# Kernel optimization log

Measured on AMD Instinct MI355X. Metric: run time of the kernel, lower is better.

## Reference

```python
import jax, jax.numpy as jnp
import numpy as np

T, N, R = 10, 50000, 50000   # time steps, nodes per graph, total restaurants
D_IN, D, H = 128, 64, 4      # input dim, hidden dim, attention heads
E = 400000                   # edges per timestep (before self-loops)
HD = D // H                  # head dim


def setup_inputs() -> dict:
    key = jax.random.key(0)
    ks = jax.random.split(key, 16)
    inp = {}
    inp["x"] = jax.random.normal(ks[0], (T, N, D_IN), jnp.float32)
    inp["edge_index"] = jax.random.randint(ks[1], (T, 2, E), 0, N, jnp.int32)
    inp["edge_weight"] = jax.random.uniform(ks[2], (T, E), jnp.float32)
    # per-timestep permutation mapping local node idx -> global restaurant idx
    inp["global_idx"] = jax.vmap(lambda k: jax.random.permutation(k, R))(
        jax.random.split(ks[3], T)).astype(jnp.int32)
    s = 0.05
    inp["gcn1_w"] = jax.random.normal(ks[4], (D, D_IN), jnp.float32) * s
    inp["gcn1_b"] = jnp.zeros((D,), jnp.float32)
    inp["gcn2_w"] = jax.random.normal(ks[5], (D, D), jnp.float32) * s
    inp["gcn2_b"] = jnp.zeros((D,), jnp.float32)
    inp["in_proj_w"] = jax.random.normal(ks[6], (3 * D, D), jnp.float32) * s
    inp["in_proj_b"] = jnp.zeros((3 * D,), jnp.float32)
    inp["out_proj_w"] = jax.random.normal(ks[7], (D, D), jnp.float32) * s
    inp["out_proj_b"] = jnp.zeros((D,), jnp.float32)
    inp["w1"] = jnp.ones((T, D), jnp.float32)
    inp["w2"] = jnp.ones((T, D), jnp.float32)
    inp["w3"] = jnp.ones((D,), jnp.float32)
    inp["w4"] = jnp.ones((D,), jnp.float32)
    inp["ln1_g"] = jnp.ones((D,), jnp.float32)
    inp["ln1_b"] = jnp.zeros((D,), jnp.float32)
    inp["ln2_g"] = jnp.ones((D,), jnp.float32)
    inp["ln2_b"] = jnp.zeros((D,), jnp.float32)
    inp["fc_w"] = jax.random.normal(ks[8], (D, D), jnp.float32) * s
    inp["fc_b"] = jnp.zeros((D,), jnp.float32)
    return inp


def _layer_norm(x, g, b, eps=1e-5):
    mu = jnp.mean(x, axis=-1, keepdims=True)
    var = jnp.mean((x - mu) ** 2, axis=-1, keepdims=True)
    return (x - mu) * jax.lax.rsqrt(var + eps) * g + b


def _gcn_layer(h, src, dst, ew, W, b):
    # PyG GCNConv with edge weights; self-loops already appended by caller.
    deg = jax.ops.segment_sum(ew, dst, num_segments=N)
    dinv = jnp.where(deg > 0, jax.lax.rsqrt(deg), 0.0)
    norm = dinv[src] * ew * dinv[dst]                      # [E+N]
    hw = h @ W.T                                           # [N, D]
    agg = jax.ops.segment_sum(norm[:, None] * hw[src], dst, num_segments=N)
    return agg + b


def _forward(x, edge_index, edge_weight, global_idx,
             gcn1_w, gcn1_b, gcn2_w, gcn2_b,
             in_proj_w, in_proj_b, out_proj_w, out_proj_b,
             w1, w2, w3, w4, ln1_g, ln1_b, ln2_g, ln2_b, fc_w, fc_b):
    loop = jnp.arange(N, dtype=edge_index.dtype)
    src = jnp.concatenate([edge_index[:, 0], jnp.broadcast_to(loop, (T, N))], axis=1)
    dst = jnp.concatenate([edge_index[:, 1], jnp.broadcast_to(loop, (T, N))], axis=1)
    ew = jnp.concatenate([edge_weight, jnp.ones((T, N), edge_weight.dtype)], axis=1)

    def per_t(xt, st, dt, wt):
        h = jax.nn.relu(_gcn_layer(xt, st, dt, wt, gcn1_w, gcn1_b))
        return jax.nn.relu(_gcn_layer(h, st, dt, wt, gcn2_w, gcn2_b))

    feat = jax.vmap(per_t)(x, src, dst, ew)                # [T, N, D]

    # scatter local features to global alignment (permutation per timestep)
    aligned = jax.vmap(lambda g, f: jnp.zeros((R, D), f.dtype).at[g].set(f))(
        global_idx, feat)                                  # [T, R, D]
    time_embeds = jnp.transpose(aligned, (1, 0, 2))        # [R, T, D]

    presence = jax.vmap(
        lambda g: jnp.zeros((R,), bool).at[g].set(True))(global_idx)  # [T, R]
    key_padding_mask = ~presence.T                          # [R, T], True = ignore
    bias = jnp.where(key_padding_mask, -1e9, 0.0)           # [R, T]

    # multi-head self-attention over time axis (batch_first, batch = R)
    qkv = time_embeds @ in_proj_w.T + in_proj_b             # [R, T, 3D]
    q, k, v = jnp.split(qkv, 3, axis=-1)
    q = q.reshape(R, T, H, HD)
    k = k.reshape(R, T, H, HD)
    v = v.reshape(R, T, H, HD)
    scores = jnp.einsum('rthd,rshd->rhts', q, k) / np.sqrt(HD)
    scores = scores + bias[:, None, None, :]
    attn = jax.nn.softmax(scores, axis=-1)                  # [R, H, T, T]
    ao = jnp.einsum('rhts,rshd->rthd', attn, v).reshape(R, T, D)
    attn_out = ao @ out_proj_w.T + out_proj_b               # [R, T, D]

    # dropouts are identity in eval mode
    time_feat = _layer_norm(w1 * time_embeds + w2 * attn_out, ln1_g, ln1_b)
    final = time_feat[:, -1, :]                             # [R, D]
    out = final @ fc_w.T + fc_b                             # [R, D]
    return _layer_norm(w3 * final + w4 * out, ln2_g, ln2_b)


def reference(x, edge_index, edge_weight, global_idx,
              gcn1_w, gcn1_b, gcn2_w, gcn2_b,
              in_proj_w, in_proj_b, out_proj_w, out_proj_b,
              w1, w2, w3, w4, ln1_g, ln1_b, ln2_g, ln2_b, fc_w, fc_b):
    return _forward(x, edge_index, edge_weight, global_idx,
                    gcn1_w, gcn1_b, gcn2_w, gcn2_b,
                    in_proj_w, in_proj_b, out_proj_w, out_proj_b,
                    w1, w2, w3, w4, ln1_g, ln1_b, ln2_g, ln2_b, fc_w, fc_b)
```

## Files before the change

kernel.cpp:

```cpp
#include <hip/hip_runtime.h>
#include <cstdint>
#include <cstddef>

namespace {

constexpr int T = 10;
constexpr int N = 50000;
constexpr int R = 50000;
constexpr int DIN = 128;
constexpr int D = 64;
constexpr int E = 400000;

constexpr int BINS = 8192;
constexpr int NR = 7;
constexpr int SEG = 16;
constexpr int ESEG = E / SEG;
constexpr int EV4 = ESEG / 4;

constexpr float WSCALE = 262144.0f;
constexpr float WINV = 1.0f / 262144.0f;

typedef __attribute__((ext_vector_type(8))) short bf16x8;
typedef __attribute__((ext_vector_type(4))) float f32x4;

__device__ __forceinline__ float bf2f(unsigned short u) {
  return __uint_as_float(((unsigned)u) << 16);
}
__device__ __forceinline__ unsigned short f2bf(float f) {
  unsigned u = __float_as_uint(f);
  return (unsigned short)((u + 0x7FFFu + ((u >> 16) & 1u)) >> 16);
}

__global__ __launch_bounds__(256) void k_hist(const int* __restrict__ ei,
                                              const float* __restrict__ ew,
                                              unsigned* __restrict__ pu) {
  __shared__ unsigned h[BINS];
  int b = blockIdx.x;
  int s = b % SEG;
  int tr = b / SEG;
  int r = tr % NR;
  int t = tr / NR;
  for (int i = threadIdx.x; i < BINS; i += 256) h[i] = 0u;
  __syncthreads();
  int bin0 = r * BINS;
  const int4* dst4 = (const int4*)(ei + (size_t)t * 2 * E + E + s * ESEG);
  const float4* ew4 = (const float4*)(ew + (size_t)t * E + s * ESEG);
  for (int i = threadIdx.x; i < EV4; i += 256) {
    int4 d = dst4[i];
    float4 w = ew4[i];
    unsigned a0 = (unsigned)(d.x - bin0);
    unsigned a1 = (unsigned)(d.y - bin0);
    unsigned a2 = (unsigned)(d.z - bin0);
    unsigned a3 = (unsigned)(d.w - bin0);
    if (a0 < (unsigned)BINS) atomicAdd(&h[a0], 0x1000000u + (unsigned)fmaf(w.x, WSCALE, 0.5f));
    if (a1 < (unsigned)BINS) atomicAdd(&h[a1], 0x1000000u + (unsigned)fmaf(w.y, WSCALE, 0.5f));
    if (a2 < (unsigned)BINS) atomicAdd(&h[a2], 0x1000000u + (unsigned)fmaf(w.z, WSCALE, 0.5f));
    if (a3 < (unsigned)BINS) atomicAdd(&h[a3], 0x1000000u + (unsigned)fmaf(w.w, WSCALE, 0.5f));
  }
  __syncthreads();
  size_t base = (size_t)b * BINS;
  for (int i = threadIdx.x; i < BINS; i += 256) pu[base + i] = h[i];
}

__global__ __launch_bounds__(256) void k_hreduce(const unsigned* __restrict__ pu,
                                                 int* __restrict__ cnt,
                                                 float* __restrict__ dinv) {
  int i = blockIdx.x * 256 + threadIdx.x;
  if (i >= T * N) return;
  int t = i / N, n = i - t * N;
  int r = n / BINS, rel = n - r * BINS;
  unsigned c = 0;
  unsigned wsum = 0;
  #pragma unroll
  for (int s = 0; s < SEG; ++s) {
    unsigned v = pu[((size_t)((t * NR + r) * SEG + s)) * BINS + rel];
    c += v >> 24;
    wsum += v & 0xFFFFFFu;
  }
  cnt[i] = (int)c;
  dinv[i] = rsqrtf(1.0f + (float)wsum * WINV);
}

__global__ __launch_bounds__(256) void k_scan(const int* __restrict__ cnt,
                                              int* __restrict__ rowptr) {
  int t = blockIdx.x;
  int lane = threadIdx.x & 63, wid = threadIdx.x >> 6;
  __shared__ int wsum[4];
  __shared__ int carry_s;
  if (threadIdx.x == 0) carry_s = 0;
  __syncthreads();
  const int4* cp = (const int4*)(cnt + (size_t)t * N);
  int4* rp = (int4*)(rowptr + (size_t)t * N);
  constexpr int NI4 = N / 4;
  for (int base = 0; base < NI4; base += 256) {
    int i = base + threadIdx.x;
    int4 v = make_int4(0, 0, 0, 0);
    if (i < NI4) v = cp[i];
    int tot = v.x + v.y + v.z + v.w;
    int s = tot;
    #pragma unroll
    for (int off = 1; off < 64; off <<= 1) {
      int u = __shfl_up(s, off, 64);
      if (lane >= off) s += u;
    }
    if (lane == 63) wsum[wid] = s;
    int carry = carry_s;
    __syncthreads();
    int wadd = 0;
    #pragma unroll
    for (int w = 0; w < 4; ++w) if (w < wid) wadd += wsum[w];
    if (i < NI4) {
      int excl = carry + wadd + s - tot;
      int4 o;
      o.x = excl;
      o.y = excl + v.x;
      o.z = o.y + v.y;
      o.w = o.z + v.z;
      rp[i] = o;
    }
    __syncthreads();
    if (threadIdx.x == 0) carry_s = carry + wsum[0] + wsum[1] + wsum[2] + wsum[3];
    __syncthreads();
  }
}

__global__ __launch_bounds__(256) void k_segoff(unsigned* __restrict__ pu,
                                                const int* __restrict__ rowptr) {
  int i = blockIdx.x * 256 + threadIdx.x;
  if (i >= T * N) return;
  int t = i / N, n = i - t * N;
  int r = n / BINS, rel = n - r * BINS;
  unsigned run = (unsigned)rowptr[i];
  #pragma unroll
  for (int s = 0; s < SEG; ++s) {
    size_t base = ((size_t)((t * NR + r) * SEG + s)) * BINS + rel;
    unsigned v = pu[base];
    pu[base] = run;
    run += v >> 24;
  }
}

__global__ __launch_bounds__(256) void k_fill2(const int* __restrict__ ei,
                                               const float* __restrict__ ew,
                                               const unsigned* __restrict__ pu,
                                               int2* __restrict__ pk) {
  __shared__ int cur[BINS];
  int b = blockIdx.x;
  int s = b % SEG;
  int tr = b / SEG;
  int r = tr % NR;
  int t = tr / NR;
  size_t pbase = (size_t)b * BINS;
  for (int i = threadIdx.x; i < BINS; i += 256) cur[i] = (int)pu[pbase + i];
  __syncthreads();
  int bin0 = r * BINS;
  const int4* src4 = (const int4*)(ei + (size_t)t * 2 * E + s * ESEG);
  const int4* dst4 = (const int4*)(ei + (size_t)t * 2 * E + E + s * ESEG);
  const float4* ew4 = (const float4*)(ew + (size_t)t * E + s * ESEG);
  int2* pkt = pk + (size_t)t * E;
  for (int i = threadIdx.x; i < EV4; i += 256) {
    int4 d = dst4[i];
    int4 sv = src4[i];
    float4 w = ew4[i];
    unsigned a0 = (unsigned)(d.x - bin0);
    unsigned a1 = (unsigned)(d.y - bin0);
    unsigned a2 = (unsigned)(d.z - bin0);
    unsigned a3 = (unsigned)(d.w - bin0);
    if (a0 < (unsigned)BINS) {
      int pos = atomicAdd(&cur[a0], 1);
      pkt[pos] = make_int2(sv.x, __float_as_int(w.x));
    }
    if (a1 < (unsigned)BINS) {
      int pos = atomicAdd(&cur[a1], 1);
      pkt[pos] = make_int2(sv.y, __float_as_int(w.y));
    }
    if (a2 < (unsigned)BINS) {
      int pos = atomicAdd(&cur[a2], 1);
      pkt[pos] = make_int2(sv.z, __float_as_int(w.z));
    }
    if (a3 < (unsigned)BINS) {
      int pos = atomicAdd(&cur[a3], 1);
      pkt[pos] = make_int2(sv.w, __float_as_int(w.w));
    }
  }
}

__global__ __launch_bounds__(256) void k_prep(const float* __restrict__ g1w,
                                              const float* __restrict__ g2w,
                                              const float* __restrict__ inw,
                                              const float* __restrict__ outw,
                                              const float* __restrict__ fcw,
                                              unsigned short* __restrict__ Wb) {
  int i = blockIdx.x * 256 + threadIdx.x;
  if (i >= 32768) return;
  const float* src;
  int off;
  if (i < 8192)       { src = g1w;  off = 0; }
  else if (i < 12288) { src = g2w;  off = 8192; }
  else if (i < 24576) { src = inw;  off = 12288; }
  else if (i < 28672) { src = outw; off = 24576; }
  else                { src = fcw;  off = 28672; }
  Wb[i] = f2bf(src[i - off]);
}

template <int K, int NT, bool BF16B, int MODE>
__global__ __launch_bounds__(256) void k_mm(const unsigned short* __restrict__ Wb,
                                            const void* __restrict__ Bv,
                                            const float* __restrict__ biasp,
                                            unsigned short* __restrict__ out,
                                            unsigned short* __restrict__ q9,
                                            int Mwaves) {
  int wv = threadIdx.x >> 6, lane = threadIdx.x & 63;
  int wave = blockIdx.x * 4 + wv;
  if (wave >= Mwaves) return;
  int m0 = wave * 16;
  int half = lane & 15, quad = lane >> 4;
  constexpr int KS = K / 32;
  int m = m0 + half;
  float ds = 1.0f;
  if (MODE == 2) ds = biasp[m];
  bf16x8 bfrag[KS];
  if (BF16B) {
    const unsigned short* Bp = (const unsigned short*)Bv + (size_t)m * K + quad * 8;
    #pragma unroll
    for (int ks = 0; ks < KS; ++ks) bfrag[ks] = *(const bf16x8*)(Bp + ks * 32);
  } else {
    const float* Bp = (const float*)Bv + (size_t)m * K + quad * 8;
    #pragma unroll
    for (int ks = 0; ks < KS; ++ks) {
      float4 f0 = *(const float4*)(Bp + ks * 32);
      float4 f1 = *(const float4*)(Bp + ks * 32 + 4);
      bf16x8 b;
      b[0] = (short)f2bf(f0.x); b[1] = (short)f2bf(f0.y);
      b[2] = (short)f2bf(f0.z); b[3] = (short)f2bf(f0.w);
      b[4] = (short)f2bf(f1.x); b[5] = (short)f2bf(f1.y);
      b[6] = (short)f2bf(f1.z); b[7] = (short)f2bf(f1.w);
      bfrag[ks] = b;
    }
  }
  #pragma unroll
  for (int jt = 0; jt < NT; ++jt) {
    f32x4 acc = {0.f, 0.f, 0.f, 0.f};
    const unsigned short* Wp = Wb + (size_t)(jt * 16 + half) * K + quad * 8;
    #pragma unroll
    for (int ks = 0; ks < KS; ++ks) {
      bf16x8 afrag = *(const bf16x8*)(Wp + ks * 32);
      acc = __builtin_amdgcn_mfma_f32_16x16x32_bf16(afrag, bfrag[ks], acc, 0, 0, 0);
    }
    int j = jt * 16 + quad * 4;
    if (MODE == 1) {
      float4 b4 = *(const float4*)(biasp + j);
      acc[0] += b4.x; acc[1] += b4.y; acc[2] += b4.z; acc[3] += b4.w;
    }
    if (MODE == 2) {
      acc[0] *= ds; acc[1] *= ds; acc[2] *= ds; acc[3] *= ds;
    }
    ushort4 o;
    o.x = f2bf(acc[0]); o.y = f2bf(acc[1]); o.z = f2bf(acc[2]); o.w = f2bf(acc[3]);
    if (MODE != 1) {
      *(ushort4*)(out + (size_t)m * (NT * 16) + j) = o;
    } else {
      if (jt < 4) {
        if (m % 10 == 9) *(ushort4*)(q9 + (size_t)(m / 10) * 64 + j) = o;
      } else {
        *(ushort4*)(out + (size_t)m * 128 + (j - 64)) = o;
      }
    }
  }
}

template <bool SCATTER>
__global__ __launch_bounds__(256) void k_gather(
    const unsigned short* __restrict__ hw, const int2* __restrict__ pk,
    const float* __restrict__ dinv, const int* __restrict__ rowptr,
    const int* __restrict__ cnt, const float* __restrict__ bias,
    const int* __restrict__ gidx, unsigned short* __restrict__ outp) {
  int wv = threadIdx.x >> 6, lane = threadIdx.x & 63;
  long long wave = (long long)blockIdx.x * 4 + wv;
  if (wave >= (long long)T * N) return;
  int t = (int)(wave / N);
  int n = (int)(wave - (long long)t * N);
  const unsigned short* hwt = hw + (size_t)t * N * D;
  const int2* pkt = pk + (size_t)t * E;
  float dn = dinv[t * N + n];
  int start = rowptr[t * N + n];
  int m = cnt[t * N + n];
  int grp = lane >> 4, sub = lane & 15;
  float4 acc0 = make_float4(0.f, 0.f, 0.f, 0.f);
  float4 acc1 = make_float4(0.f, 0.f, 0.f, 0.f);
  for (int b = 0; b < m; b += 64) {
    int mm = min(64, m - b);
    int2 rec = make_int2(0, 0);
    if (lane < mm) rec = pkt[start + b + lane];
    int s_l = rec.x;
    float w_l = __int_as_float(rec.y);
    int iters = (mm + 3) >> 2;
    int i = 0;
    for (; i + 2 <= iters; i += 2) {
      int i0 = 4 * i + grp;
      int i1 = i0 + 4;
      int sa = __shfl(s_l, i0, 64);
      float wa = __shfl(w_l, i0, 64);
      int sb = __shfl(s_l, i1, 64);
      float wb = __shfl(w_l, i1, 64);
      ushort4 ha = *(const ushort4*)(hwt + (size_t)sa * D + (sub << 2));
      ushort4 hb = *(const ushort4*)(hwt + (size_t)sb * D + (sub << 2));
      acc0.x = fmaf(wa, bf2f(ha.x), acc0.x);
      acc0.y = fmaf(wa, bf2f(ha.y), acc0.y);
      acc0.z = fmaf(wa, bf2f(ha.z), acc0.z);
      acc0.w = fmaf(wa, bf2f(ha.w), acc0.w);
      acc1.x = fmaf(wb, bf2f(hb.x), acc1.x);
      acc1.y = fmaf(wb, bf2f(hb.y), acc1.y);
      acc1.z = fmaf(wb, bf2f(hb.z), acc1.z);
      acc1.w = fmaf(wb, bf2f(hb.w), acc1.w);
    }
    if (i < iters) {
      int i0 = 4 * i + grp;
      int sa = __shfl(s_l, i0, 64);
      float wa = __shfl(w_l, i0, 64);
      ushort4 ha = *(const ushort4*)(hwt + (size_t)sa * D + (sub << 2));
      acc0.x = fmaf(wa, bf2f(ha.x), acc0.x);
      acc0.y = fmaf(wa, bf2f(ha.y), acc0.y);
      acc0.z = fmaf(wa, bf2f(ha.z), acc0.z);
      acc0.w = fmaf(wa, bf2f(ha.w), acc0.w);
    }
  }
  acc0.x += acc1.x; acc0.y += acc1.y; acc0.z += acc1.z; acc0.w += acc1.w;
  acc0.x += __shfl_xor(acc0.x, 16, 64); acc0.x += __shfl_xor(acc0.x, 32, 64);
  acc0.y += __shfl_xor(acc0.y, 16, 64); acc0.y += __shfl_xor(acc0.y, 32, 64);
  acc0.z += __shfl_xor(acc0.z, 16, 64); acc0.z += __shfl_xor(acc0.z, 32, 64);
  acc0.w += __shfl_xor(acc0.w, 16, 64); acc0.w += __shfl_xor(acc0.w, 32, 64);
  if (grp == 0) {
    ushort4 sv = *(const ushort4*)(hwt + (size_t)n * D + (sub << 2));
    float4 b4 = *(const float4*)(bias + (sub << 2));
    float vx = fmaxf(fmaf(dn, acc0.x + bf2f(sv.x), b4.x), 0.f);
    float vy = fmaxf(fmaf(dn, acc0.y + bf2f(sv.y), b4.y), 0.f);
    float vz = fmaxf(fmaf(dn, acc0.z + bf2f(sv.z), b4.z), 0.f);
    float vw = fmaxf(fmaf(dn, acc0.w + bf2f(sv.w), b4.w), 0.f);
    ushort4 o;
    o.x = f2bf(vx); o.y = f2bf(vy); o.z = f2bf(vz); o.w = f2bf(vw);
    size_t ro;
    if (SCATTER) {
      int rr = gidx[(size_t)t * R + n];
      ro = ((size_t)rr * T + t) * D;
    } else {
      ro = ((size_t)t * N + n) * D;
    }
    *(ushort4*)(outp + ro + (sub << 2)) = o;
  }
}

__global__ __launch_bounds__(256) void k_attn2(const unsigned short* __restrict__ kv,
                                               const unsigned short* __restrict__ q9,
                                               unsigned short* __restrict__ ao) {
  int wv = threadIdx.x >> 6, lane = threadIdx.x & 63;
  int r = blockIdx.x * 4 + wv;
  if (r >= R) return;
  float qv = bf2f(q9[(size_t)r * 64 + lane]);
  const unsigned short* kvr = kv + (size_t)r * T * 128;
  float sc[T], vv[T];
  #pragma unroll
  for (int s = 0; s < T; ++s) {
    float kk = bf2f(kvr[s * 128 + lane]);
    vv[s] = bf2f(kvr[s * 128 + 64 + lane]);
    float p = qv * kk;
    p += __shfl_xor(p, 8, 16);
    p += __shfl_xor(p, 4, 16);
    p += __shfl_xor(p, 2, 16);
    p += __shfl_xor(p, 1, 16);
    sc[s] = p * 0.25f;
  }
  float mx = sc[0];
  #pragma unroll
  for (int s = 1; s < T; ++s) mx = fmaxf(mx, sc[s]);
  float ssum = 0.f;
  #pragma unroll
  for (int s = 0; s < T; ++s) { sc[s] = expf(sc[s] - mx); ssum += sc[s]; }
  float rinv = 1.0f / ssum;
  float aov = 0.f;
  #pragma unroll
  for (int s = 0; s < T; ++s) aov = fmaf(sc[s] * rinv, vv[s], aov);
  ao[(size_t)r * 64 + lane] = f2bf(aov);
}

__global__ __launch_bounds__(256) void k_ln1(const unsigned short* __restrict__ te,
                                             const unsigned short* __restrict__ proj,
                                             const float* __restrict__ outB,
                                             const float* __restrict__ w1,
                                             const float* __restrict__ w2,
                                             const float* __restrict__ g1,
                                             const float* __restrict__ b1,
                                             float* __restrict__ finf,
                                             unsigned short* __restrict__ finb) {
  int wv = threadIdx.x >> 6, lane = threadIdx.x & 63;
  int r = blockIdx.x * 4 + wv;
  if (r >= R) return;
  float t9 = bf2f(te[((size_t)r * T + (T - 1)) * 64 + lane]);
  float pr = bf2f(proj[(size_t)r * 64 + lane]) + outB[lane];
  float pre = w1[(T - 1) * 64 + lane] * t9 + w2[(T - 1) * 64 + lane] * pr;
  float s1 = pre;
  #pragma unroll
  for (int off = 32; off >= 1; off >>= 1) s1 += __shfl_xor(s1, off, 64);
  float mu = s1 * (1.0f / 64.0f);
  float dv = pre - mu;
  float s2 = dv * dv;
  #pragma unroll
  for (int off = 32; off >= 1; off >>= 1) s2 += __shfl_xor(s2, off, 64);
  float rstd = 1.0f / sqrtf(s2 * (1.0f / 64.0f) + 1e-5f);
  float fin = dv * rstd * g1[lane] + b1[lane];
  finf[(size_t)r * 64 + lane] = fin;
  finb[(size_t)r * 64 + lane] = f2bf(fin);
}

__global__ __launch_bounds__(256) void k_ln2(const float* __restrict__ finf,
                                             const unsigned short* __restrict__ o2,
                                             const float* __restrict__ fcB,
                                             const float* __restrict__ w3,
                                             const float* __restrict__ w4,
                                             const float* __restrict__ g2,
                                             const float* __restrict__ b2,
                                             float* __restrict__ out) {
  int wv = threadIdx.x >> 6, lane = threadIdx.x & 63;
  int r = blockIdx.x * 4 + wv;
  if (r >= R) return;
  float fin = finf[(size_t)r * 64 + lane];
  float oo = bf2f(o2[(size_t)r * 64 + lane]) + fcB[lane];
  float pre = w3[lane] * fin + w4[lane] * oo;
  float s1 = pre;
  #pragma unroll
  for (int off = 32; off >= 1; off >>= 1) s1 += __shfl_xor(s1, off, 64);
  float mu = s1 * (1.0f / 64.0f);
  float dv = pre - mu;
  float s2 = dv * dv;
  #pragma unroll
  for (int off = 32; off >= 1; off >>= 1) s2 += __shfl_xor(s2, off, 64);
  float rstd = 1.0f / sqrtf(s2 * (1.0f / 64.0f) + 1e-5f);
  out[(size_t)r * 64 + lane] = dv * rstd * g2[lane] + b2[lane];
}

}

extern "C" void kernel_launch(void* const* d_in, const int* in_sizes, int n_in,
                              void* d_out, int out_size, void* d_ws, size_t ws_size,
                              hipStream_t stream) {
  const float* x      = (const float*)d_in[0];
  const int*   ei     = (const int*)d_in[1];
  const float* ew     = (const float*)d_in[2];
  const int*   gidx   = (const int*)d_in[3];
  const float* gcn1_w = (const float*)d_in[4];
  const float* gcn1_b = (const float*)d_in[5];
  const float* gcn2_w = (const float*)d_in[6];
  const float* gcn2_b = (const float*)d_in[7];
  const float* in_w   = (const float*)d_in[8];
  const float* in_b   = (const float*)d_in[9];
  const float* out_w  = (const float*)d_in[10];
  const float* out_b  = (const float*)d_in[11];
  const float* w1     = (const float*)d_in[12];
  const float* w2     = (const float*)d_in[13];
  const float* w3     = (const float*)d_in[14];
  const float* w4     = (const float*)d_in[15];
  const float* ln1_g  = (const float*)d_in[16];
  const float* ln1_b  = (const float*)d_in[17];
  const float* ln2_g  = (const float*)d_in[18];
  const float* ln2_b  = (const float*)d_in[19];
  const float* fc_w   = (const float*)d_in[20];
  const float* fc_b   = (const float*)d_in[21];
  float* outp = (float*)d_out;

  char* ws = (char*)d_ws;
  size_t off = 0;
  auto alloc = [&](size_t bytes) {
    void* p = ws + off;
    off += (bytes + 255) & ~(size_t)255;
    return p;
  };
  unsigned short* h1te = (unsigned short*)alloc(sizeof(short) * (size_t)T * N * D);
  unsigned short* q9b  = (unsigned short*)alloc(sizeof(short) * (size_t)R * D);
  unsigned short* aob  = (unsigned short*)alloc(sizeof(short) * (size_t)R * D);
  unsigned short* proj = (unsigned short*)alloc(sizeof(short) * (size_t)R * D);
  float*          finf = (float*)alloc(sizeof(float) * (size_t)R * D);
  unsigned short* finb = (unsigned short*)alloc(sizeof(short) * (size_t)R * D);
  unsigned short* o2b  = (unsigned short*)alloc(sizeof(short) * (size_t)R * D);
  unsigned short* Wb   = (unsigned short*)alloc(sizeof(short) * 32768);
  size_t u_base = off;
  float* dinv   = (float*)alloc(sizeof(float) * T * N);
  int*   cnt    = (int*)alloc(sizeof(int) * T * N);
  int*   rowptr = (int*)alloc(sizeof(int) * T * N);
  int2*  pk     = (int2*)alloc(sizeof(int2) * (size_t)T * E);
  size_t pu_off = off;
  unsigned* pu  = (unsigned*)alloc(sizeof(unsigned) * (size_t)T * NR * SEG * BINS);
  unsigned short* hw = (unsigned short*)(ws + pu_off);
  size_t hw_end = pu_off + sizeof(short) * (size_t)T * N * D;
  if (hw_end > off) off = hw_end;
  unsigned short* kv = (unsigned short*)(ws + u_base);
  size_t kv_end = u_base + sizeof(short) * (size_t)T * N * 128;
  if (kv_end > off) off = kv_end;

  const unsigned short* W1b = Wb;
  const unsigned short* W2b = Wb + 8192;
  const unsigned short* WIb = Wb + 12288;
  const unsigned short* WOb = Wb + 24576;
  const unsigned short* WFb = Wb + 28672;

  const int M = T * N;
  const int MW = M / 16;
  const int RW = R / 16;
  const int PREP_BLOCKS = T * NR * SEG;

  k_hist<<<PREP_BLOCKS, 256, 0, stream>>>(ei, ew, pu);
  k_hreduce<<<(T * N + 255) / 256, 256, 0, stream>>>(pu, cnt, dinv);
  k_scan<<<T, 256, 0, stream>>>(cnt, rowptr);
  k_segoff<<<(T * N + 255) / 256, 256, 0, stream>>>(pu, rowptr);
  k_fill2<<<PREP_BLOCKS, 256, 0, stream>>>(ei, ew, pu, pk);
  k_prep<<<128, 256, 0, stream>>>(gcn1_w, gcn2_w, in_w, out_w, fc_w, Wb);

  k_mm<DIN, 4, false, 2><<<(MW + 3) / 4, 256, 0, stream>>>(W1b, x, dinv, hw, nullptr, MW);
  k_gather<false><<<(M + 3) / 4, 256, 0, stream>>>(hw, pk, dinv, rowptr, cnt, gcn1_b,
                                                   nullptr, h1te);
  k_mm<D, 4, true, 2><<<(MW + 3) / 4, 256, 0, stream>>>(W2b, h1te, dinv, hw, nullptr, MW);
  k_gather<true><<<(M + 3) / 4, 256, 0, stream>>>(hw, pk, dinv, rowptr, cnt, gcn2_b,
                                                  gidx, h1te);

  k_mm<D, 12, true, 1><<<(MW + 3) / 4, 256, 0, stream>>>(WIb, h1te, in_b, kv, q9b, MW);
  k_attn2<<<(R + 3) / 4, 256, 0, stream>>>(kv, q9b, aob);
  k_mm<D, 4, true, 0><<<(RW + 3) / 4, 256, 0, stream>>>(WOb, aob, nullptr, proj, nullptr, RW);
  k_ln1<<<(R + 3) / 4, 256, 0, stream>>>(h1te, proj, out_b, w1, w2, ln1_g, ln1_b, finf, finb);
  k_mm<D, 4, true, 0><<<(RW + 3) / 4, 256, 0, stream>>>(WFb, finb, nullptr, o2b, nullptr, RW);
  k_ln2<<<(R + 3) / 4, 256, 0, stream>>>(finf, o2b, fc_b, w3, w4, ln2_g, ln2_b, outp);
}
```

Before: 1.211 ms.

## Switch intermediates to fp16 and restructure GCN gather to 8 edges per wave

Replaces every bf16 intermediate and MFMA with fp16, which removes the manual round-to-nearest conversion code in favour of native conversions. The gather kernel is rewritten so each wave processes 8 edges at a time, each lane loading 16 bytes per edge row. Partial sums are reduced through shared memory instead of shuffles, and the grid becomes 2D by (node, timestep). fp16 has a narrower exponent range than bf16, so large activations could overflow. The shared-memory reduction relies only on a wave barrier within each wave.

```diff
diff --git a/kernel.cpp b/kernel.cpp
--- a/kernel.cpp
+++ b/kernel.cpp
@@ -20,16 +20,10 @@
 constexpr float WSCALE = 262144.0f;
 constexpr float WINV = 1.0f / 262144.0f;
 
-typedef __attribute__((ext_vector_type(8))) short bf16x8;
+typedef _Float16 h16;
+typedef __attribute__((ext_vector_type(8))) _Float16 f16x8;
+typedef __attribute__((ext_vector_type(4))) _Float16 f16x4;
 typedef __attribute__((ext_vector_type(4))) float f32x4;
-
-__device__ __forceinline__ float bf2f(unsigned short u) {
-  return __uint_as_float(((unsigned)u) << 16);
-}
-__device__ __forceinline__ unsigned short f2bf(float f) {
-  unsigned u = __float_as_uint(f);
-  return (unsigned short)((u + 0x7FFFu + ((u >> 16) & 1u)) >> 16);
-}
 
 __global__ __launch_bounds__(256) void k_hist(const int* __restrict__ ei,
                                               const float* __restrict__ ew,
@@ -190,7 +184,7 @@
                                               const float* __restrict__ inw,
                                               const float* __restrict__ outw,
                                               const float* __restrict__ fcw,
-                                              unsigned short* __restrict__ Wb) {
+                                              h16* __restrict__ Wb) {
   int i = blockIdx.x * 256 + threadIdx.x;
   if (i >= 32768) return;
   const float* src;
@@ -200,15 +194,15 @@
   else if (i < 24576) { src = inw;  off = 12288; }
   else if (i < 28672) { src = outw; off = 24576; }
   else                { src = fcw;  off = 28672; }
-  Wb[i] = f2bf(src[i - off]);
-}
-
-template <int K, int NT, bool BF16B, int MODE>
-__global__ __launch_bounds__(256) void k_mm(const unsigned short* __restrict__ Wb,
+  Wb[i] = (h16)src[i - off];
+}
+
+template <int K, int NT, bool F16B, int MODE>
+__global__ __launch_bounds__(256) void k_mm(const h16* __restrict__ Wb,
                                             const void* __restrict__ Bv,
                                             const float* __restrict__ biasp,
-                                            unsigned short* __restrict__ out,
-                                            unsigned short* __restrict__ q9,
+                                            h16* __restrict__ out,
+                                            h16* __restrict__ q9,
                                             int Mwaves) {
   int wv = threadIdx.x >> 6, lane = threadIdx.x & 63;
   int wave = blockIdx.x * 4 + wv;
@@ -219,33 +213,31 @@
   int m = m0 + half;
   float ds = 1.0f;
   if (MODE == 2) ds = biasp[m];
-  bf16x8 bfrag[KS];
-  if (BF16B) {
-    const unsigned short* Bp = (const unsigned short*)Bv + (size_t)m * K + quad * 8;
-    #pragma unroll
-    for (int ks = 0; ks < KS; ++ks) bfrag[ks] = *(const bf16x8*)(Bp + ks * 32);
+  f16x8 bfrag[KS];
+  if (F16B) {
+    const h16* Bp = (const h16*)Bv + (size_t)m * K + quad * 8;
+    #pragma unroll
+    for (int ks = 0; ks < KS; ++ks) bfrag[ks] = *(const f16x8*)(Bp + ks * 32);
   } else {
     const float* Bp = (const float*)Bv + (size_t)m * K + quad * 8;
     #pragma unroll
     for (int ks = 0; ks < KS; ++ks) {
       float4 f0 = *(const float4*)(Bp + ks * 32);
       float4 f1 = *(const float4*)(Bp + ks * 32 + 4);
-      bf16x8 b;
-      b[0] = (short)f2bf(f0.x); b[1] = (short)f2bf(f0.y);
-      b[2] = (short)f2bf(f0.z); b[3] = (short)f2bf(f0.w);
-      b[4] = (short)f2bf(f1.x); b[5] = (short)f2bf(f1.y);
-      b[6] = (short)f2bf(f1.z); b[7] = (short)f2bf(f1.w);
+      f16x8 b;
+      b[0] = (h16)f0.x; b[1] = (h16)f0.y; b[2] = (h16)f0.z; b[3] = (h16)f0.w;
+      b[4] = (h16)f1.x; b[5] = (h16)f1.y; b[6] = (h16)f1.z; b[7] = (h16)f1.w;
       bfrag[ks] = b;
     }
   }
   #pragma unroll
   for (int jt = 0; jt < NT; ++jt) {
     f32x4 acc = {0.f, 0.f, 0.f, 0.f};
-    const unsigned short* Wp = Wb + (size_t)(jt * 16 + half) * K + quad * 8;
+    const h16* Wp = Wb + (size_t)(jt * 16 + half) * K + quad * 8;
     #pragma unroll
     for (int ks = 0; ks < KS; ++ks) {
-      bf16x8 afrag = *(const bf16x8*)(Wp + ks * 32);
-      acc = __builtin_amdgcn_mfma_f32_16x16x32_bf16(afrag, bfrag[ks], acc, 0, 0, 0);
+      f16x8 afrag = *(const f16x8*)(Wp + ks * 32);
+      acc = __builtin_amdgcn_mfma_f32_16x16x32_f16(afrag, bfrag[ks], acc, 0, 0, 0);
     }
     int j = jt * 16 + quad * 4;
     if (MODE == 1) {
@@ -255,15 +247,15 @@
     if (MODE == 2) {
       acc[0] *= ds; acc[1] *= ds; acc[2] *= ds; acc[3] *= ds;
     }
-    ushort4 o;
-    o.x = f2bf(acc[0]); o.y = f2bf(acc[1]); o.z = f2bf(acc[2]); o.w = f2bf(acc[3]);
+    f16x4 o;
+    o[0] = (h16)acc[0]; o[1] = (h16)acc[1]; o[2] = (h16)acc[2]; o[3] = (h16)acc[3];
     if (MODE != 1) {
-      *(ushort4*)(out + (size_t)m * (NT * 16) + j) = o;
+      *(f16x4*)(out + (size_t)m * (NT * 16) + j) = o;
     } else {
       if (jt < 4) {
-        if (m % 10 == 9) *(ushort4*)(q9 + (size_t)(m / 10) * 64 + j) = o;
+        if (m % 10 == 9) *(f16x4*)(q9 + (size_t)(m / 10) * 64 + j) = o;
       } else {
-        *(ushort4*)(out + (size_t)m * 128 + (j - 64)) = o;
+        *(f16x4*)(out + (size_t)m * 128 + (j - 64)) = o;
       }
     }
   }
@@ -271,98 +263,64 @@
 
 template <bool SCATTER>
 __global__ __launch_bounds__(256) void k_gather(
-    const unsigned short* __restrict__ hw, const int2* __restrict__ pk,
+    const h16* __restrict__ hw, const int2* __restrict__ pk,
     const float* __restrict__ dinv, const int* __restrict__ rowptr,
     const int* __restrict__ cnt, const float* __restrict__ bias,
-    const int* __restrict__ gidx, unsigned short* __restrict__ outp) {
+    const int* __restrict__ gidx, h16* __restrict__ outp) {
+  __shared__ float red[4][8][64];
   int wv = threadIdx.x >> 6, lane = threadIdx.x & 63;
-  long long wave = (long long)blockIdx.x * 4 + wv;
-  if (wave >= (long long)T * N) return;
-  int t = (int)(wave / N);
-  int n = (int)(wave - (long long)t * N);
-  const unsigned short* hwt = hw + (size_t)t * N * D;
+  int t = blockIdx.y;
+  int n = blockIdx.x * 4 + wv;
+  const h16* hwt = hw + (size_t)t * N * D;
   const int2* pkt = pk + (size_t)t * E;
   float dn = dinv[t * N + n];
   int start = rowptr[t * N + n];
   int m = cnt[t * N + n];
-  int grp = lane >> 4, sub = lane & 15;
-  float4 acc0 = make_float4(0.f, 0.f, 0.f, 0.f);
-  float4 acc1 = make_float4(0.f, 0.f, 0.f, 0.f);
-  for (int b = 0; b < m; b += 64) {
-    int mm = min(64, m - b);
-    int2 rec = make_int2(0, 0);
-    if (lane < mm) rec = pkt[start + b + lane];
-    int s_l = rec.x;
-    float w_l = __int_as_float(rec.y);
-    int iters = (mm + 3) >> 2;
-    int i = 0;
-    for (; i + 2 <= iters; i += 2) {
-      int i0 = 4 * i + grp;
-      int i1 = i0 + 4;
-      int sa = __shfl(s_l, i0, 64);
-      float wa = __shfl(w_l, i0, 64);
-      int sb = __shfl(s_l, i1, 64);
-      float wb = __shfl(w_l, i1, 64);
-      ushort4 ha = *(const ushort4*)(hwt + (size_t)sa * D + (sub << 2));
-      ushort4 hb = *(const ushort4*)(hwt + (size_t)sb * D + (sub << 2));
-      acc0.x = fmaf(wa, bf2f(ha.x), acc0.x);
-      acc0.y = fmaf(wa, bf2f(ha.y), acc0.y);
-      acc0.z = fmaf(wa, bf2f(ha.z), acc0.z);
-      acc0.w = fmaf(wa, bf2f(ha.w), acc0.w);
-      acc1.x = fmaf(wb, bf2f(hb.x), acc1.x);
-      acc1.y = fmaf(wb, bf2f(hb.y), acc1.y);
-      acc1.z = fmaf(wb, bf2f(hb.z), acc1.z);
-      acc1.w = fmaf(wb, bf2f(hb.w), acc1.w);
-    }
-    if (i < iters) {
-      int i0 = 4 * i + grp;
-      int sa = __shfl(s_l, i0, 64);
-      float wa = __shfl(w_l, i0, 64);
-      ushort4 ha = *(const ushort4*)(hwt + (size_t)sa * D + (sub << 2));
-      acc0.x = fmaf(wa, bf2f(ha.x), acc0.x);
-      acc0.y = fmaf(wa, bf2f(ha.y), acc0.y);
-      acc0.z = fmaf(wa, bf2f(ha.z), acc0.z);
-      acc0.w = fmaf(wa, bf2f(ha.w), acc0.w);
-    }
-  }
-  acc0.x += acc1.x; acc0.y += acc1.y; acc0.z += acc1.z; acc0.w += acc1.w;
-  acc0.x += __shfl_xor(acc0.x, 16, 64); acc0.x += __shfl_xor(acc0.x, 32, 64);
-  acc0.y += __shfl_xor(acc0.y, 16, 64); acc0.y += __shfl_xor(acc0.y, 32, 64);
-  acc0.z += __shfl_xor(acc0.z, 16, 64); acc0.z += __shfl_xor(acc0.z, 32, 64);
-  acc0.w += __shfl_xor(acc0.w, 16, 64); acc0.w += __shfl_xor(acc0.w, 32, 64);
-  if (grp == 0) {
-    ushort4 sv = *(const ushort4*)(hwt + (size_t)n * D + (sub << 2));
-    float4 b4 = *(const float4*)(bias + (sub << 2));
-    float vx = fmaxf(fmaf(dn, acc0.x + bf2f(sv.x), b4.x), 0.f);
-    float vy = fmaxf(fmaf(dn, acc0.y + bf2f(sv.y), b4.y), 0.f);
-    float vz = fmaxf(fmaf(dn, acc0.z + bf2f(sv.z), b4.z), 0.f);
-    float vw = fmaxf(fmaf(dn, acc0.w + bf2f(sv.w), b4.w), 0.f);
-    ushort4 o;
-    o.x = f2bf(vx); o.y = f2bf(vy); o.z = f2bf(vz); o.w = f2bf(vw);
-    size_t ro;
-    if (SCATTER) {
-      int rr = gidx[(size_t)t * R + n];
-      ro = ((size_t)rr * T + t) * D;
-    } else {
-      ro = ((size_t)t * N + n) * D;
-    }
-    *(ushort4*)(outp + ro + (sub << 2)) = o;
-  }
-}
-
-__global__ __launch_bounds__(256) void k_attn2(const unsigned short* __restrict__ kv,
-                                               const unsigned short* __restrict__ q9,
-                                               unsigned short* __restrict__ ao) {
+  int grp = lane >> 3, sub = lane & 7;
+  f32x4 accL = {0.f, 0.f, 0.f, 0.f};
+  f32x4 accH = {0.f, 0.f, 0.f, 0.f};
+  for (int e = grp; e < m; e += 8) {
+    int2 rec = pkt[start + e];
+    float w = __int_as_float(rec.y);
+    f16x8 h = *(const f16x8*)(hwt + (size_t)rec.x * D + sub * 8);
+    #pragma unroll
+    for (int j = 0; j < 4; ++j) accL[j] = fmaf(w, (float)h[j], accL[j]);
+    #pragma unroll
+    for (int j = 0; j < 4; ++j) accH[j] = fmaf(w, (float)h[j + 4], accH[j]);
+  }
+  float* rw = &red[wv][grp][sub * 8];
+  *(f32x4*)(rw) = accL;
+  *(f32x4*)(rw + 4) = accH;
+  __builtin_amdgcn_wave_barrier();
+  const float* rr = &red[wv][0][lane];
+  float s = 0.f;
+  #pragma unroll
+  for (int g = 0; g < 8; ++g) s += rr[g * 64];
+  float selfv = (float)hwt[(size_t)n * D + lane];
+  float v = fmaxf(fmaf(dn, s + selfv, bias[lane]), 0.f);
+  size_t ro;
+  if (SCATTER) {
+    int rr2 = gidx[(size_t)t * R + n];
+    ro = ((size_t)rr2 * T + t) * D + lane;
+  } else {
+    ro = ((size_t)t * N + n) * D + lane;
+  }
+  outp[ro] = (h16)v;
+}
+
+__global__ __launch_bounds__(256) void k_attn2(const h16* __restrict__ kv,
+                                               const h16* __restrict__ q9,
+                                               h16* __restrict__ ao) {
   int wv = threadIdx.x >> 6, lane = threadIdx.x & 63;
   int r = blockIdx.x * 4 + wv;
   if (r >= R) return;
-  float qv = bf2f(q9[(size_t)r * 64 + lane]);
-  const unsigned short* kvr = kv + (size_t)r * T * 128;
+  float qv = (float)q9[(size_t)r * 64 + lane];
+  const h16* kvr = kv + (size_t)r * T * 128;
   float sc[T], vv[T];
   #pragma unroll
   for (int s = 0; s < T; ++s) {
-    float kk = bf2f(kvr[s * 128 + lane]);
-    vv[s] = bf2f(kvr[s * 128 + 64 + lane]);
+    float kk = (float)kvr[s * 128 + lane];
+    vv[s] = (float)kvr[s * 128 + 64 + lane];
     float p = qv * kk;
     p += __shfl_xor(p, 8, 16);
     p += __shfl_xor(p, 4, 16);
@@ -380,23 +338,23 @@
   float aov = 0.f;
   #pragma unroll
   for (int s = 0; s < T; ++s) aov = fmaf(sc[s] * rinv, vv[s], aov);
-  ao[(size_t)r * 64 + lane] = f2bf(aov);
-}
-
-__global__ __launch_bounds__(256) void k_ln1(const unsigned short* __restrict__ te,
-                                             const unsigned short* __restrict__ proj,
+  ao[(size_t)r * 64 + lane] = (h16)aov;
+}
+
+__global__ __launch_bounds__(256) void k_ln1(const h16* __restrict__ te,
+                                             const h16* __restrict__ proj,
                                              const float* __restrict__ outB,
                                              const float* __restrict__ w1,
                                              const float* __restrict__ w2,
                                              const float* __restrict__ g1,
                                              const float* __restrict__ b1,
                                              float* __restrict__ finf,
-                                             unsigned short* __restrict__ finb) {
+                                             h16* __restrict__ finb) {
   int wv = threadIdx.x >> 6, lane = threadIdx.x & 63;
   int r = blockIdx.x * 4 + wv;
   if (r >= R) return;
-  float t9 = bf2f(te[((size_t)r * T + (T - 1)) * 64 + lane]);
-  float pr = bf2f(proj[(size_t)r * 64 + lane]) + outB[lane];
+  float t9 = (float)te[((size_t)r * T + (T - 1)) * 64 + lane];
+  float pr = (float)proj[(size_t)r * 64 + lane] + outB[lane];
   float pre = w1[(T - 1) * 64 + lane] * t9 + w2[(T - 1) * 64 + lane] * pr;
   float s1 = pre;
   #pragma unroll
@@ -409,11 +367,11 @@
   float rstd = 1.0f / sqrtf(s2 * (1.0f / 64.0f) + 1e-5f);
   float fin = dv * rstd * g1[lane] + b1[lane];
   finf[(size_t)r * 64 + lane] = fin;
-  finb[(size_t)r * 64 + lane] = f2bf(fin);
+  finb[(size_t)r * 64 + lane] = (h16)fin;
 }
 
 __global__ __launch_bounds__(256) void k_ln2(const float* __restrict__ finf,
-                                             const unsigned short* __restrict__ o2,
+                                             const h16* __restrict__ o2,
                                              const float* __restrict__ fcB,
                                              const float* __restrict__ w3,
                                              const float* __restrict__ w4,
@@ -424,7 +382,7 @@
   int r = blockIdx.x * 4 + wv;
   if (r >= R) return;
   float fin = finf[(size_t)r * 64 + lane];
-  float oo = bf2f(o2[(size_t)r * 64 + lane]) + fcB[lane];
+  float oo = (float)o2[(size_t)r * 64 + lane] + fcB[lane];
   float pre = w3[lane] * fin + w4[lane] * oo;
   float s1 = pre;
   #pragma unroll
@@ -474,14 +432,14 @@
     off += (bytes + 255) & ~(size_t)255;
     return p;
   };
-  unsigned short* h1te = (unsigned short*)alloc(sizeof(short) * (size_t)T * N * D);
-  unsigned short* q9b  = (unsigned short*)alloc(sizeof(short) * (size_t)R * D);
-  unsigned short* aob  = (unsigned short*)alloc(sizeof(short) * (size_t)R * D);
-  unsigned short* proj = (unsigned short*)alloc(sizeof(short) * (size_t)R * D);
-  float*          finf = (float*)alloc(sizeof(float) * (size_t)R * D);
-  unsigned short* finb = (unsigned short*)alloc(sizeof(short) * (size_t)R * D);
-  unsigned short* o2b  = (unsigned short*)alloc(sizeof(short) * (size_t)R * D);
-  unsigned short* Wb   = (unsigned short*)alloc(sizeof(short) * 32768);
+  h16* h1te = (h16*)alloc(sizeof(h16) * (size_t)T * N * D);
+  h16* q9b  = (h16*)alloc(sizeof(h16) * (size_t)R * D);
+  h16* aob  = (h16*)alloc(sizeof(h16) * (size_t)R * D);
+  h16* proj = (h16*)alloc(sizeof(h16) * (size_t)R * D);
+  float* finf = (float*)alloc(sizeof(float) * (size_t)R * D);
+  h16* finb = (h16*)alloc(sizeof(h16) * (size_t)R * D);
+  h16* o2b  = (h16*)alloc(sizeof(h16) * (size_t)R * D);
+  h16* Wb   = (h16*)alloc(sizeof(h16) * 32768);
   size_t u_base = off;
   float* dinv   = (float*)alloc(sizeof(float) * T * N);
   int*   cnt    = (int*)alloc(sizeof(int) * T * N);
@@ -489,18 +447,18 @@
   int2*  pk     = (int2*)alloc(sizeof(int2) * (size_t)T * E);
   size_t pu_off = off;
   unsigned* pu  = (unsigned*)alloc(sizeof(unsigned) * (size_t)T * NR * SEG * BINS);
-  unsigned short* hw = (unsigned short*)(ws + pu_off);
-  size_t hw_end = pu_off + sizeof(short) * (size_t)T * N * D;
+  h16* hw = (h16*)(ws + pu_off);
+  size_t hw_end = pu_off + sizeof(h16) * (size_t)T * N * D;
   if (hw_end > off) off = hw_end;
-  unsigned short* kv = (unsigned short*)(ws + u_base);
-  size_t kv_end = u_base + sizeof(short) * (size_t)T * N * 128;
+  h16* kv = (h16*)(ws + u_base);
+  size_t kv_end = u_base + sizeof(h16) * (size_t)T * N * 128;
   if (kv_end > off) off = kv_end;
 
-  const unsigned short* W1b = Wb;
-  const unsigned short* W2b = Wb + 8192;
-  const unsigned short* WIb = Wb + 12288;
-  const unsigned short* WOb = Wb + 24576;
-  const unsigned short* WFb = Wb + 28672;
+  const h16* W1b = Wb;
+  const h16* W2b = Wb + 8192;
+  const h16* WIb = Wb + 12288;
+  const h16* WOb = Wb + 24576;
+  const h16* WFb = Wb + 28672;
 
   const int M = T * N;
   const int MW = M / 16;
@@ -514,12 +472,11 @@
   k_fill2<<<PREP_BLOCKS, 256, 0, stream>>>(ei, ew, pu, pk);
   k_prep<<<128, 256, 0, stream>>>(gcn1_w, gcn2_w, in_w, out_w, fc_w, Wb);
 
+  dim3 gg(N / 4, T);
   k_mm<DIN, 4, false, 2><<<(MW + 3) / 4, 256, 0, stream>>>(W1b, x, dinv, hw, nullptr, MW);
-  k_gather<false><<<(M + 3) / 4, 256, 0, stream>>>(hw, pk, dinv, rowptr, cnt, gcn1_b,
-                                                   nullptr, h1te);
+  k_gather<false><<<gg, 256, 0, stream>>>(hw, pk, dinv, rowptr, cnt, gcn1_b, nullptr, h1te);
   k_mm<D, 4, true, 2><<<(MW + 3) / 4, 256, 0, stream>>>(W2b, h1te, dinv, hw, nullptr, MW);
-  k_gather<true><<<(M + 3) / 4, 256, 0, stream>>>(hw, pk, dinv, rowptr, cnt, gcn2_b,
-                                                  gidx, h1te);
+  k_gather<true><<<gg, 256, 0, stream>>>(hw, pk, dinv, rowptr, cnt, gcn2_b, gidx, h1te);
 
   k_mm<D, 12, true, 1><<<(MW + 3) / 4, 256, 0, stream>>>(WIb, h1te, in_b, kv, q9b, MW);
   k_attn2<<<(R + 3) / 4, 256, 0, stream>>>(kv, q9b, aob);
```

After: 1.194 ms. Within noise of the previous version (-1.4%).
